# Performance work log

Hardware: AMD Instinct MI355X
Metric: run time of the kernel (lower is better)

Reference implementation:

```python
import jax, jax.numpy as jnp
import numpy as np

B, CIN, N = 4, 128, 4096
CKEY, COUT = 64, 128

def setup_inputs() -> dict:
    key = jax.random.key(0)
    k1, k2, k3, k4 = jax.random.split(key, 4)
    x = jax.random.normal(k1, (B, CIN, N), dtype=jnp.float32)
    # Conv1d(kernel_size=1, bias=False) weights as [out, in] matrices
    Wq = jax.random.normal(k2, (CKEY, CIN), dtype=jnp.float32) * (1.0 / np.sqrt(CIN))
    Wk = jax.random.normal(k3, (CKEY, CIN), dtype=jnp.float32) * (1.0 / np.sqrt(CIN))
    Wv = jax.random.normal(k4, (COUT, CIN), dtype=jnp.float32) * (1.0 / np.sqrt(CIN))
    return {"x": x, "Wq": Wq, "Wk": Wk, "Wv": Wv}

def reference(x, Wq, Wk, Wv):
    # 1x1 conv projections: [B, C, N] -> [B, C', N]
    Q = jnp.einsum('ki,bin->bkn', Wq, x)   # [B, CKEY, N]
    K = jnp.einsum('ki,bin->bkn', Wk, x)   # [B, CKEY, N]
    V = jnp.einsum('oi,bin->bon', Wv, x)   # [B, COUT, N]
    # A = softmax(Q^T K) over last dim -- NOTE: no 1/sqrt(d) scaling, as in original
    scores = jnp.einsum('bkn,bkm->bnm', Q, K)     # [B, N, N]
    A = jax.nn.softmax(scores, axis=2)
    # out = (A @ V^T)^T -> [B, COUT, N]
    out = jnp.einsum('bnm,bom->bon', A, V)
    return out
```

## Files before the change

### kernel.cpp

```cpp
#include <hip/hip_runtime.h>
#include <hip/hip_bf16.h>

#define NN    4096
#define BB    4
#define CIN_  128
#define COUT_ 128

typedef __attribute__((ext_vector_type(8))) short bf16x8;
typedef __attribute__((ext_vector_type(4))) short bf16x4;
typedef __attribute__((ext_vector_type(4))) float f32x4;
typedef __attribute__((ext_vector_type(2))) int   i32x2;

#define MFMA16 __builtin_amdgcn_mfma_f32_16x16x32_bf16
#define SWK(row, g) ((((row) << 6)) + ((((g) ^ ((row) & 7))) << 3))

__device__ __forceinline__ float bf2f(short s) {
    union { unsigned int u; float f; } c; c.u = ((unsigned int)(unsigned short)s) << 16; return c.f;
}
__device__ __forceinline__ short f2bf(float f) {
    union { float f; unsigned int u; } c; c.f = f;
    unsigned int r = c.u + 0x7fffu + ((c.u >> 16) & 1u);
    return (short)(r >> 16);
}
__device__ __forceinline__ float fexp2(float x) {
#if __has_builtin(__builtin_amdgcn_exp2f)
    return __builtin_amdgcn_exp2f(x);
#else
    return exp2f(x);
#endif
}
__device__ __forceinline__ unsigned int pack_bf16(float a, float b) {
    union { float f; unsigned int u; } ca, cb; ca.f = a; cb.f = b;
    unsigned int ua = ca.u + 0x8000u, ub = cb.u + 0x8000u;
#if __has_builtin(__builtin_amdgcn_perm)
    return __builtin_amdgcn_perm(ub, ua, 0x07060302u);
#else
    return (ua >> 16) | (ub & 0xffff0000u);
#endif
}

__global__ __launch_bounds__(256) void proj_kernel(const float* __restrict__ x,
                                                   const float* __restrict__ Wq,
                                                   const float* __restrict__ Wk,
                                                   const float* __restrict__ Wv,
                                                   short* __restrict__ Qh, short* __restrict__ Ql,
                                                   short* __restrict__ Kh, short* __restrict__ Kl,
                                                   short* __restrict__ Vb) {
    __shared__ __align__(16) short xsh[16 * 64 * 8];
    __shared__ __align__(16) short xsl[16 * 64 * 8];

    int tid  = threadIdx.x;
    int b    = blockIdx.y;
    int gz   = blockIdx.z;
    int gn0  = blockIdx.x * 64;
    int wave = tid >> 6;
    int lane = tid & 63;
    int quad = lane >> 4;
    int l15  = lane & 15;

    const float* xb = x + (size_t)b * CIN_ * NN + gn0;
#pragma unroll
    for (int rep = 0; rep < 4; ++rep) {
        int slot = rep * 256 + tid;
        int c = slot >> 6, n = slot & 63;
        bf16x8 h8, l8;
#pragma unroll
        for (int j = 0; j < 8; ++j) {
            float f = xb[(c * 8 + j) * NN + n];
            short h = f2bf(f);
            h8[j] = h;
            l8[j] = f2bf(f - bf2f(h));
        }
        *(bf16x8*)(xsh + (c * 64 + n) * 8) = h8;
        *(bf16x8*)(xsl + (c * 64 + n) * 8) = l8;
    }
    __syncthreads();

    int rg = gz * 4 + wave;

    const float* wrow;
    float scale = 1.0f;
    if (rg < 4)      { wrow = Wq + (rg * 16 + l15) * CIN_; scale = 1.4426950408889634f; }
    else if (rg < 8) { wrow = Wk + ((rg - 4) * 16 + l15) * CIN_; }
    else             { wrow = Wv + ((rg - 8) * 16 + l15) * CIN_; }

    bf16x8 wh[4], wl[4];
#pragma unroll
    for (int kc = 0; kc < 4; ++kc) {
        const float* wp = wrow + kc * 32 + quad * 8;
#pragma unroll
        for (int j = 0; j < 8; ++j) {
            float w = wp[j] * scale;
            short h = f2bf(w);
            wh[kc][j] = h;
            wl[kc][j] = f2bf(w - bf2f(h));
        }
    }

    f32x4 acc[4];
#pragma unroll
    for (int ct = 0; ct < 4; ++ct) acc[ct] = (f32x4){0.f, 0.f, 0.f, 0.f};

#pragma unroll
    for (int kc = 0; kc < 4; ++kc) {
#pragma unroll
        for (int ct = 0; ct < 4; ++ct) {
            bf16x8 xh = *(const bf16x8*)(xsh + (((kc * 4 + quad) * 64) + ct * 16 + l15) * 8);
            bf16x8 xl = *(const bf16x8*)(xsl + (((kc * 4 + quad) * 64) + ct * 16 + l15) * 8);
            acc[ct] = MFMA16(wh[kc], xh, acc[ct], 0, 0, 0);
            acc[ct] = MFMA16(wh[kc], xl, acc[ct], 0, 0, 0);
            acc[ct] = MFMA16(wl[kc], xh, acc[ct], 0, 0, 0);
        }
    }

    if (rg < 8) {
        short* H = (rg < 4) ? Qh : Kh;
        short* L = (rg < 4) ? Ql : Kl;
        int rb    = (rg < 4) ? rg : (rg - 4);
        int chunk = rb * 2 + (quad >> 1);
        int sub   = (quad & 1) * 4;
#pragma unroll
        for (int ct = 0; ct < 4; ++ct) {
            int n = gn0 + ct * 16 + l15;
            bf16x4 h4, l4;
#pragma unroll
            for (int r = 0; r < 4; ++r) {
                float f = acc[ct][r];
                short h = f2bf(f);
                h4[r] = h;
                l4[r] = f2bf(f - bf2f(h));
            }
            *(bf16x4*)(H + (((b * 8 + chunk) * NN) + n) * 8 + sub) = h4;
            *(bf16x4*)(L + (((b * 8 + chunk) * NN) + n) * 8 + sub) = l4;
        }
    } else {
        int o0 = rg * 16 + quad * 4 - 128;
#pragma unroll
        for (int ct = 0; ct < 4; ++ct) {
            int n = gn0 + ct * 16 + l15;
#pragma unroll
            for (int r = 0; r < 4; ++r)
                Vb[((size_t)(b * COUT_ + o0 + r)) * NN + n] = f2bf(acc[ct][r]);
        }
    }
}

__global__ __launch_bounds__(256, 2) void flash_kernel(const short* __restrict__ Qh,
                                                       const short* __restrict__ Ql,
                                                       const short* __restrict__ Kh,
                                                       const short* __restrict__ Kl,
                                                       const short* __restrict__ Vb,
                                                       float* __restrict__ outp,
                                                       short* __restrict__ opart,
                                                       float* __restrict__ lsum,
                                                       int S, int direct) {
    __shared__ __align__(16) short VT[128 * 64];
    __shared__ __align__(16) short PW[4 * 32 * 64];

    int tid  = threadIdx.x;
    int bx   = blockIdx.x;
    int b    = bx / S;
    int s    = bx - b * S;
    int qt   = blockIdx.y;
    int wave = tid >> 6;
    int lane = tid & 63;
    int quad = lane >> 4;
    int l15  = lane & 15;

    int nq0 = qt * 128 + wave * 32 + l15;
    bf16x8 qh0[2], qh1[2], ql0[2], ql1[2];
#pragma unroll
    for (int u = 0; u < 2; ++u) {
        int nq = nq0 + u * 16;
        qh0[u] = *(const bf16x8*)(Qh + (((b * 8 + quad)     * NN) + nq) * 8);
        qh1[u] = *(const bf16x8*)(Qh + (((b * 8 + 4 + quad) * NN) + nq) * 8);
        ql0[u] = *(const bf16x8*)(Ql + (((b * 8 + quad)     * NN) + nq) * 8);
        ql1[u] = *(const bf16x8*)(Ql + (((b * 8 + 4 + quad) * NN) + nq) * 8);
    }

    f32x4 O[2][8];
#pragma unroll
    for (int u = 0; u < 2; ++u)
#pragma unroll
        for (int f = 0; f < 8; ++f) O[u][f] = (f32x4){0.f, 0.f, 0.f, 0.f};
    float lp[2] = {0.f, 0.f};

    int vrow = tid & 127, vc0 = (tid >> 7) * 4;
    short* pwb = PW + wave * 2048;

    int KPS   = NN / S;
    int kb    = s * KPS;
    int iters = KPS / 64;

    const short* KhB = Kh + (size_t)b * 8 * NN * 8;
    const short* KlB = Kl + (size_t)b * 8 * NN * 8;
    const short* VbB = Vb + (size_t)b * COUT_ * NN;

    bf16x8 nv[4];
#pragma unroll
    for (int q = 0; q < 4; ++q)
        nv[q] = *(const bf16x8*)(VbB + (size_t)vrow * NN + kb + (vc0 + q) * 8);

    for (int it = 0; it < iters; ++it) {
        bf16x8 kh0[4], kh1[4], kl0[4], kl1[4];
#pragma unroll
        for (int f = 0; f < 4; ++f) {
            int row = kb + f * 16 + l15;
            kh0[f] = *(const bf16x8*)(KhB + ((quad       * NN) + row) * 8);
            kh1[f] = *(const bf16x8*)(KhB + (((4 + quad) * NN) + row) * 8);
            kl0[f] = *(const bf16x8*)(KlB + ((quad       * NN) + row) * 8);
            kl1[f] = *(const bf16x8*)(KlB + (((4 + quad) * NN) + row) * 8);
        }

#pragma unroll
        for (int q = 0; q < 4; ++q)
            *(bf16x8*)(VT + SWK(vrow, vc0 + q)) = nv[q];
        __syncthreads();

        if (it + 1 < iters) {
            int nb = kb + 64;
#pragma unroll
            for (int q = 0; q < 4; ++q)
                nv[q] = *(const bf16x8*)(VbB + (size_t)vrow * NN + nb + (vc0 + q) * 8);
        }

        f32x4 sA[2][4];
#pragma unroll
        for (int f = 0; f < 4; ++f) {
#pragma unroll
            for (int u = 0; u < 2; ++u) {
                f32x4 acc = (f32x4){0.f, 0.f, 0.f, 0.f};
                acc = MFMA16(kh0[f], qh0[u], acc, 0, 0, 0);
                acc = MFMA16(kh1[f], qh1[u], acc, 0, 0, 0);
                acc = MFMA16(kl0[f], qh0[u], acc, 0, 0, 0);
                acc = MFMA16(kl1[f], qh1[u], acc, 0, 0, 0);
                acc = MFMA16(kh0[f], ql0[u], acc, 0, 0, 0);
                acc = MFMA16(kh1[f], ql1[u], acc, 0, 0, 0);
                sA[u][f] = acc;
            }
        }

#pragma unroll
        for (int u = 0; u < 2; ++u) {
            int row = u * 16 + l15;
#pragma unroll
            for (int f = 0; f < 4; ++f) {
                float p0 = fexp2(sA[u][f][0]);
                float p1 = fexp2(sA[u][f][1]);
                float p2 = fexp2(sA[u][f][2]);
                float p3 = fexp2(sA[u][f][3]);
                lp[u] += (p0 + p1) + (p2 + p3);
                unsigned int w0 = pack_bf16(p0, p1);
                unsigned int w1 = pack_bf16(p2, p3);
                *(i32x2*)(pwb + SWK(row, f * 2 + (quad >> 1)) + (quad & 1) * 4) =
                    (i32x2){(int)w0, (int)w1};
            }
        }

#pragma unroll
        for (int g = 0; g < 2; ++g) {
            bf16x8 pb0 = *(const bf16x8*)(pwb + SWK(l15,      g * 4 + quad));
            bf16x8 pb1 = *(const bf16x8*)(pwb + SWK(16 + l15, g * 4 + quad));
#pragma unroll
            for (int f8 = 0; f8 < 8; ++f8) {
                bf16x8 vA = *(const bf16x8*)(VT + SWK(f8 * 16 + l15, g * 4 + quad));
                O[0][f8] = MFMA16(vA, pb0, O[0][f8], 0, 0, 0);
                O[1][f8] = MFMA16(vA, pb1, O[1][f8], 0, 0, 0);
            }
        }
        __syncthreads();
        kb += 64;
    }

#pragma unroll
    for (int u = 0; u < 2; ++u) {
        lp[u] += __shfl_xor(lp[u], 16, 64);
        lp[u] += __shfl_xor(lp[u], 32, 64);
    }

#pragma unroll
    for (int u = 0; u < 2; ++u) {
        int n = nq0 + u * 16;
        if (direct) {
            float inv = 1.f / lp[u];
#pragma unroll
            for (int f8 = 0; f8 < 8; ++f8)
#pragma unroll
                for (int r = 0; r < 4; ++r) {
                    int o = f8 * 16 + quad * 4 + r;
                    outp[((size_t)(b * COUT_ + o)) * NN + n] = O[u][f8][r] * inv;
                }
        } else {
#pragma unroll
            for (int f8 = 0; f8 < 8; ++f8)
#pragma unroll
                for (int r = 0; r < 4; ++r) {
                    int o = f8 * 16 + quad * 4 + r;
                    opart[((size_t)((b * S + s) * COUT_ + o)) * NN + n] = f2bf(O[u][f8][r]);
                }
            if (quad == 0) lsum[(b * S + s) * NN + n] = lp[u];
        }
    }
}

__global__ __launch_bounds__(256, 4) void merge_kernel(const short* __restrict__ Opart,
                                                       const float* __restrict__ lsum,
                                                       float* __restrict__ out, int S) {
    int idx = blockIdx.x * 256 + threadIdx.x;
    int n0  = (idx & (NN / 4 - 1)) * 4;
    int rest = idx >> 10;
    int o = rest & (COUT_ - 1);
    int b = rest >> 7;

    f32x4 den = (f32x4){0.f, 0.f, 0.f, 0.f};
    f32x4 acc = (f32x4){0.f, 0.f, 0.f, 0.f};
    for (int s = 0; s < S; ++s) {
        f32x4 l  = *(const f32x4*)(lsum + (b * S + s) * NN + n0);
        bf16x4 ov = *(const bf16x4*)(Opart + ((size_t)((b * S + s) * COUT_ + o)) * NN + n0);
#pragma unroll
        for (int j = 0; j < 4; ++j) {
            den[j] += l[j];
            acc[j] += bf2f(ov[j]);
        }
    }
    f32x4 res;
#pragma unroll
    for (int j = 0; j < 4; ++j) res[j] = acc[j] / den[j];
    *(f32x4*)(out + ((size_t)(b * COUT_ + o)) * NN + n0) = res;
}

extern "C" void kernel_launch(void* const* d_in, const int* in_sizes, int n_in,
                              void* d_out, int out_size, void* d_ws, size_t ws_size,
                              hipStream_t stream) {
    const float* x  = (const float*)d_in[0];
    const float* Wq = (const float*)d_in[1];
    const float* Wk = (const float*)d_in[2];
    const float* Wv = (const float*)d_in[3];

    char* ws = (char*)d_ws;
    short* Qh = (short*)ws;
    short* Ql = Qh + 1048576;
    short* Kh = Ql + 1048576;
    short* Kl = Kh + 1048576;
    short* Vb = Kl + 1048576;
    size_t base = 4ull * 2097152 + 4194304;
    const size_t MLSZ  = (size_t)BB * NN * 4;
    const size_t OPB   = (size_t)BB * COUT_ * NN * 2;

    int S;
    if      (ws_size >= base + 8 * (MLSZ + OPB)) S = 8;
    else if (ws_size >= base + 4 * (MLSZ + OPB)) S = 4;
    else                                         S = 1;
    int direct = (S == 1);

    float* lsum  = (float*)(ws + base);
    short* Opart = (short*)(ws + base + (size_t)S * MLSZ);

    proj_kernel<<<dim3(NN / 64, BB, 4), 256, 0, stream>>>(x, Wq, Wk, Wv, Qh, Ql, Kh, Kl, Vb);
    flash_kernel<<<dim3(BB * S, NN / 128), 256, 0, stream>>>(
        Qh, Ql, Kh, Kl, Vb, (float*)d_out, Opart, lsum, S, direct);
    if (!direct)
        merge_kernel<<<BB * COUT_ * NN / 4 / 256, 256, 0, stream>>>(Opart, lsum, (float*)d_out, S);
}
```

Baseline: 132.3 us.

## Stream V tiles into double-buffered LDS via global_load_lds and use 4-way KV split

The V tile is now copied from global memory straight into LDS with async global_load_lds, using two LDS buffers. The next tile's load overlaps the current iteration's compute, and the per-iteration register-staged copy into LDS plus the trailing barrier go away. The XOR swizzle is reproduced by permuting source addresses per lane. The split over the key dimension also drops from 8 to 4 whenever workspace allows, which halves the grid and the merge work in exchange for fewer blocks in flight. LDS use per block doubles for V, which may affect occupancy.

```diff
diff --git a/kernel.cpp b/kernel.cpp
--- a/kernel.cpp
+++ b/kernel.cpp
@@ -37,6 +37,11 @@
 #else
     return (ua >> 16) | (ub & 0xffff0000u);
 #endif
+}
+__device__ __forceinline__ void gll16(const short* g, short* l) {
+    __builtin_amdgcn_global_load_lds(
+        (const __attribute__((address_space(1))) void*)g,
+        (__attribute__((address_space(3))) void*)l, 16, 0, 0);
 }
 
 __global__ __launch_bounds__(256) void proj_kernel(const float* __restrict__ x,
@@ -154,7 +159,7 @@
                                                        short* __restrict__ opart,
                                                        float* __restrict__ lsum,
                                                        int S, int direct) {
-    __shared__ __align__(16) short VT[128 * 64];
+    __shared__ __align__(16) short VT[2 * 128 * 64];
     __shared__ __align__(16) short PW[4 * 32 * 64];
 
     int tid  = threadIdx.x;
@@ -166,6 +171,8 @@
     int lane = tid & 63;
     int quad = lane >> 4;
     int l15  = lane & 15;
+    int l8   = lane >> 3;
+    int l7   = lane & 7;
 
     int nq0 = qt * 128 + wave * 32 + l15;
     bf16x8 qh0[2], qh1[2], ql0[2], ql1[2];
@@ -185,7 +192,6 @@
         for (int f = 0; f < 8; ++f) O[u][f] = (f32x4){0.f, 0.f, 0.f, 0.f};
     float lp[2] = {0.f, 0.f};
 
-    int vrow = tid & 127, vc0 = (tid >> 7) * 4;
     short* pwb = PW + wave * 2048;
 
     int KPS   = NN / S;
@@ -196,12 +202,17 @@
     const short* KlB = Kl + (size_t)b * 8 * NN * 8;
     const short* VbB = Vb + (size_t)b * COUT_ * NN;
 
-    bf16x8 nv[4];
-#pragma unroll
-    for (int q = 0; q < 4; ++q)
-        nv[q] = *(const bf16x8*)(VbB + (size_t)vrow * NN + kb + (vc0 + q) * 8);
-
+    const short* vsrc = VbB + (size_t)(wave * 8 + l8) * NN + (l7 ^ l8) * 8;
+    int vdst = wave * 512;
+
+#pragma unroll
+    for (int j = 0; j < 4; ++j)
+        gll16(vsrc + (size_t)j * 32 * NN + kb, VT + vdst + j * 2048);
+
+    int cur = 0;
     for (int it = 0; it < iters; ++it) {
+        __syncthreads();
+
         bf16x8 kh0[4], kh1[4], kl0[4], kl1[4];
 #pragma unroll
         for (int f = 0; f < 4; ++f) {
@@ -212,16 +223,12 @@
             kl1[f] = *(const bf16x8*)(KlB + (((4 + quad) * NN) + row) * 8);
         }
 
-#pragma unroll
-        for (int q = 0; q < 4; ++q)
-            *(bf16x8*)(VT + SWK(vrow, vc0 + q)) = nv[q];
-        __syncthreads();
-
         if (it + 1 < iters) {
             int nb = kb + 64;
-#pragma unroll
-            for (int q = 0; q < 4; ++q)
-                nv[q] = *(const bf16x8*)(VbB + (size_t)vrow * NN + nb + (vc0 + q) * 8);
+            short* vb1 = VT + ((cur ^ 1) << 13) + vdst;
+#pragma unroll
+            for (int j = 0; j < 4; ++j)
+                gll16(vsrc + (size_t)j * 32 * NN + nb, vb1 + j * 2048);
         }
 
         f32x4 sA[2][4];
@@ -257,18 +264,21 @@
             }
         }
 
-#pragma unroll
-        for (int g = 0; g < 2; ++g) {
-            bf16x8 pb0 = *(const bf16x8*)(pwb + SWK(l15,      g * 4 + quad));
-            bf16x8 pb1 = *(const bf16x8*)(pwb + SWK(16 + l15, g * 4 + quad));
-#pragma unroll
-            for (int f8 = 0; f8 < 8; ++f8) {
-                bf16x8 vA = *(const bf16x8*)(VT + SWK(f8 * 16 + l15, g * 4 + quad));
-                O[0][f8] = MFMA16(vA, pb0, O[0][f8], 0, 0, 0);
-                O[1][f8] = MFMA16(vA, pb1, O[1][f8], 0, 0, 0);
+        {
+            const short* vt = VT + (cur << 13);
+#pragma unroll
+            for (int g = 0; g < 2; ++g) {
+                bf16x8 pb0 = *(const bf16x8*)(pwb + SWK(l15,      g * 4 + quad));
+                bf16x8 pb1 = *(const bf16x8*)(pwb + SWK(16 + l15, g * 4 + quad));
+#pragma unroll
+                for (int f8 = 0; f8 < 8; ++f8) {
+                    bf16x8 vA = *(const bf16x8*)(vt + SWK(f8 * 16 + l15, g * 4 + quad));
+                    O[0][f8] = MFMA16(vA, pb0, O[0][f8], 0, 0, 0);
+                    O[1][f8] = MFMA16(vA, pb1, O[1][f8], 0, 0, 0);
+                }
             }
         }
-        __syncthreads();
+        cur ^= 1;
         kb += 64;
     }
 
@@ -348,9 +358,8 @@
     const size_t OPB   = (size_t)BB * COUT_ * NN * 2;
 
     int S;
-    if      (ws_size >= base + 8 * (MLSZ + OPB)) S = 8;
-    else if (ws_size >= base + 4 * (MLSZ + OPB)) S = 4;
-    else                                         S = 1;
+    if (ws_size >= base + 4 * (MLSZ + OPB)) S = 4;
+    else                                    S = 1;
     int direct = (S == 1);
 
     float* lsum  = (float*)(ws + base);
```

Result: faster. 124.4 us (-6.0%).
